# Kernel tuning notes

Hardware: AMD Instinct MI355X
Metric: run time of the kernel (lower is better)

## Reference

```python
import jax, jax.numpy as jnp
import numpy as np

PRE_NMS_TOPN = 6000   # cfg.TEST.RPN_PRE_NMS_TOP_N
POST_NMS_TOPN = 1000  # cfg.TEST.RPN_POST_NMS_TOP_N
NMS_THRESH = 0.7      # cfg.TEST.RPN_NMS_THRESH
MIN_SIZE = 0.0        # cfg.TEST.RPN_MIN_SIZE
BBOX_XFORM_CLIP = float(np.log(1000.0 / 16.0))
FEAT_STRIDE = 8.0     # 1 / spatial_scale


def _generate_anchors(base_size=16, ratios=(0.5, 1.0, 2.0), scales=(2, 4, 8, 16, 32)):
    """Standard Detectron anchor generation -> (A, 4) = (15, 4)."""
    def whctrs(a):
        w = a[2] - a[0] + 1.0
        h = a[3] - a[1] + 1.0
        return w, h, a[0] + 0.5 * (w - 1.0), a[1] + 0.5 * (h - 1.0)

    def mk(ws, hs, xc, yc):
        ws = ws[:, None]; hs = hs[:, None]
        return np.hstack([xc - 0.5 * (ws - 1.0), yc - 0.5 * (hs - 1.0),
                          xc + 0.5 * (ws - 1.0), yc + 0.5 * (hs - 1.0)])

    base = np.array([0.0, 0.0, base_size - 1.0, base_size - 1.0])
    w, h, xc, yc = whctrs(base)
    rs = np.array(ratios)
    ws = np.round(np.sqrt(w * h / rs))
    hs = np.round(ws * rs)
    ratio_anchors = mk(ws, hs, xc, yc)
    out = []
    for a in ratio_anchors:
        w, h, xc, yc = whctrs(a)
        sc = np.array(scales, dtype=np.float64)
        out.append(mk(w * sc, h * sc, xc, yc))
    return np.vstack(out).astype(np.float32)


def _proposals_one_image(all_anchors, im_info, bbox_deltas, scores):
    # bbox_deltas: (4A, H, W), scores: (A, H, W)
    deltas = bbox_deltas.transpose(1, 2, 0).reshape(-1, 4)  # (K*A, 4)
    s = scores.transpose(1, 2, 0).reshape(-1)               # (K*A,)

    # pre-NMS top-k by objectness (argpartition+argsort in original)
    top_s, order = jax.lax.top_k(s, PRE_NMS_TOPN)
    d = deltas[order]
    anc = all_anchors[order]

    # bbox_transform with weights (1,1,1,1) and dw/dh clipping
    ws = anc[:, 2] - anc[:, 0] + 1.0
    hs = anc[:, 3] - anc[:, 1] + 1.0
    cx = anc[:, 0] + 0.5 * ws
    cy = anc[:, 1] + 0.5 * hs
    dx, dy = d[:, 0], d[:, 1]
    dw = jnp.minimum(d[:, 2], BBOX_XFORM_CLIP)
    dh = jnp.minimum(d[:, 3], BBOX_XFORM_CLIP)
    pcx = dx * ws + cx
    pcy = dy * hs + cy
    pw = jnp.exp(dw) * ws
    ph = jnp.exp(dh) * hs
    x1 = pcx - 0.5 * pw
    y1 = pcy - 0.5 * ph
    x2 = pcx + 0.5 * pw - 1.0
    y2 = pcy + 0.5 * ph - 1.0

    # clip_tiled_boxes to image extent
    h_im, w_im, scale = im_info[0], im_info[1], im_info[2]
    x1 = jnp.clip(x1, 0.0, w_im - 1.0)
    y1 = jnp.clip(y1, 0.0, h_im - 1.0)
    x2 = jnp.clip(x2, 0.0, w_im - 1.0)
    y2 = jnp.clip(y2, 0.0, h_im - 1.0)
    boxes = jnp.stack([x1, y1, x2, y2], axis=1)  # (PRE, 4)

    # _filter_boxes -> validity mask (replaces gather-by-keep)
    bws = x2 - x1 + 1.0
    bhs = y2 - y1 + 1.0
    min_sz = MIN_SIZE * scale
    valid = (bws >= min_sz) & (bhs >= min_sz) & ((x1 + bws / 2.0) < w_im) & ((y1 + bhs / 2.0) < h_im)

    # greedy NMS on score-sorted boxes (boxes already sorted descending)
    areas = bws * bhs
    ix1 = jnp.maximum(x1[:, None], x1[None, :])
    iy1 = jnp.maximum(y1[:, None], y1[None, :])
    ix2 = jnp.minimum(x2[:, None], x2[None, :])
    iy2 = jnp.minimum(y2[:, None], y2[None, :])
    inter = jnp.maximum(ix2 - ix1 + 1.0, 0.0) * jnp.maximum(iy2 - iy1 + 1.0, 0.0)
    iou = inter / (areas[:, None] + areas[None, :] - inter)

    later = jnp.arange(PRE_NMS_TOPN)

    def body(i, keep):
        sup = keep[i] & (iou[i] > NMS_THRESH) & (later > i)
        return keep & ~sup

    keep = jax.lax.fori_loop(0, PRE_NMS_TOPN, body, valid)

    # fixed-size output: top POST_NMS_TOPN surviving boxes, padded (score=-1, box=0)
    masked = jnp.where(keep, top_s, -1.0)
    out_s, idx = jax.lax.top_k(masked, POST_NMS_TOPN)
    pad = (out_s > -1.0).astype(boxes.dtype)
    out_b = boxes[idx] * pad[:, None]
    return out_b, out_s


def reference(rpn_cls_prob, rpn_bbox_pred, im_info, anchors):
    N, A, H, W = rpn_cls_prob.shape
    dt = rpn_bbox_pred.dtype
    shift_x = jnp.arange(W, dtype=dt) * FEAT_STRIDE
    shift_y = jnp.arange(H, dtype=dt) * FEAT_STRIDE
    # torch.meshgrid default 'ij' ordering (faithful to original)
    sx, sy = jnp.meshgrid(shift_x, shift_y, indexing='ij')  # (W, H)
    shifts = jnp.stack([sx.ravel(), sy.ravel(), sx.ravel(), sy.ravel()], axis=1)  # (K, 4)
    all_anchors = (anchors[None, :, :] + shifts[:, None, :]).reshape(-1, 4)  # (K*A, 4)

    boxes, probs = jax.vmap(_proposals_one_image, in_axes=(None, 0, 0, 0))(
        all_anchors, im_info, rpn_bbox_pred, rpn_cls_prob)
    batch_inds = jnp.broadcast_to(jnp.arange(N, dtype=boxes.dtype)[:, None, None],
                                  (N, POST_NMS_TOPN, 1))
    rois = jnp.concatenate([batch_inds, boxes], axis=-1).reshape(-1, 5)
    return rois, probs.reshape(-1)


def setup_inputs() -> dict:
    key = jax.random.key(0)
    k1, k2 = jax.random.split(key)
    N, A, H, W = 2, 15, 128, 128
    rpn_cls_prob = jax.random.uniform(k1, (N, A, H, W), dtype=jnp.float32)
    rpn_bbox_pred = jax.random.normal(k2, (N, 4 * A, H, W), dtype=jnp.float32) * 0.2
    im_info = jnp.tile(jnp.array([[1024.0, 1024.0, 1.0]], dtype=jnp.float32), (N, 1))
    anchors = jnp.asarray(_generate_anchors())
    return {"rpn_cls_prob": rpn_cls_prob, "rpn_bbox_pred": rpn_bbox_pred,
            "im_info": im_info, "anchors": anchors}
```

## Files before the change

kernel.cpp:

```cpp
#include <hip/hip_runtime.h>
#include <hip/hip_bf16.h>

#define A_NUM 15
#define HDIM 128
#define WDIM 128
#define HW (HDIM*WDIM)
#define PER_IMG (A_NUM*HW)
#define NIMG 2
#define PRE_N 6000
#define POST_N 1000
#define NBLK 94
#define NPAD (NBLK*64)
#define SORTN 8192
#define CHUNK4 4096
#define NBIN 16384
#define HPART 16
#define PROD_T 448
#define WPT 14

typedef unsigned long long ull;

#define META_OFF   0u
#define HIST_OFF   64u
#define SEL_OFF    131136u
#define BOX_OFF    262208u
#define VALIDW_OFF 550976u
#define MASK_OFF   553024u

__device__ __forceinline__ unsigned int f2ord(float f) {
    unsigned int u = __float_as_uint(f);
    return (u & 0x80000000u) ? ~u : (u | 0x80000000u);
}
__device__ __forceinline__ float ord2f(unsigned int u) {
    unsigned int s = (u & 0x80000000u) ? (u ^ 0x80000000u) : ~u;
    return __uint_as_float(s);
}
__device__ __forceinline__ ull readlane64(ull v, int l) {
    unsigned int lo = (unsigned int)__builtin_amdgcn_readlane((int)(unsigned int)v, l);
    unsigned int hi = (unsigned int)__builtin_amdgcn_readlane((int)(unsigned int)(v >> 32), l);
    return ((ull)hi << 32) | lo;
}
__device__ __forceinline__ void barrier_lds() {
    asm volatile("s_waitcnt lgkmcnt(0)" ::: "memory");
    __builtin_amdgcn_s_barrier();
    asm volatile("" ::: "memory");
}

__global__ __launch_bounds__(1024) void k_hist16(const float* __restrict__ cls,
                                                 unsigned int* __restrict__ hist) {
    __shared__ unsigned int h[NBIN];
    int img = blockIdx.y, part = blockIdx.x;
    int t = threadIdx.x;
    for (int b = t; b < NBIN; b += 1024) h[b] = 0;
    __syncthreads();
    int base = img * PER_IMG + part * (PER_IMG / HPART);
    for (int e = t; e < PER_IMG / HPART; e += 1024) {
        unsigned int u = f2ord(cls[base + e]);
        unsigned int bin = (u >> 16) - 0x8000u;
        if (bin > (NBIN - 1)) bin = NBIN - 1;
        atomicAdd(&h[bin], 1u);
    }
    __syncthreads();
    unsigned int* hp = hist + (size_t)img * NBIN;
    for (int b = t; b < NBIN; b += 1024)
        if (h[b]) atomicAdd(&hp[b], h[b]);
}

__global__ __launch_bounds__(1024) void k_scan16(const unsigned int* __restrict__ hist,
                                                 unsigned int* __restrict__ meta) {
    __shared__ unsigned int csum[1024];
    __shared__ unsigned int aux[64];
    __shared__ unsigned int binv[16];
    int img = blockIdx.x, t = threadIdx.x;
    const unsigned int* hp = hist + (size_t)img * NBIN;
    unsigned int s = 0;
    #pragma unroll
    for (int q = 0; q < 16; ++q) s += hp[t * 16 + q];
    csum[t] = s;
    __syncthreads();
    if (t < 64) {
        unsigned int x = 0;
        #pragma unroll
        for (int q = 0; q < 16; ++q) x += csum[t * 16 + q];
        aux[t] = x;
    }
    __syncthreads();
    if (t < 64) {
        unsigned int suf = 0;
        for (int q = t; q < 64; ++q) suf += aux[q];
        ull mb1 = __ballot(suf >= PRE_N);
        int sstar = 63 - __clzll(mb1);
        unsigned int sufnext = (unsigned)__shfl((int)suf, (sstar + 1) & 63);
        unsigned int cumAbove = (sstar == 63) ? 0u : sufnext;
        unsigned int sufC = 0;
        if (t < 16) {
            for (int q = sstar * 16 + t; q < sstar * 16 + 16; ++q) sufC += csum[q];
            sufC += cumAbove;
        }
        ull mb2 = __ballot((t < 16) && (sufC >= PRE_N));
        int crel = 63 - __clzll(mb2);
        int cstar = sstar * 16 + crel;
        unsigned int cumAbove2 = (crel == 15) ? cumAbove : (unsigned)__shfl((int)sufC, crel + 1);
        if (t < 16) binv[t] = hp[cstar * 16 + t];
        unsigned int sufB = 0;
        if (t < 16) {
            for (int q = t; q < 16; ++q) sufB += binv[q];
            sufB += cumAbove2;
        }
        ull mb3 = __ballot((t < 16) && (sufB >= PRE_N));
        int brel = 63 - __clzll(mb3);
        if (t == 0) {
            meta[2 + img] = (unsigned)(cstar * 16 + brel) + 0x8000u;
            meta[img] = 0u;
        }
    }
}

__global__ __launch_bounds__(256) void k_gather(const float* __restrict__ cls,
                                                unsigned int* __restrict__ meta,
                                                ull* __restrict__ selkeys) {
    __shared__ unsigned int lcnt[NIMG], lbase[NIMG];
    int t = threadIdx.x;
    int tid = blockIdx.x * 256 + t;
    if (t < NIMG) lcnt[t] = 0;
    __syncthreads();
    unsigned int T0 = meta[2], T1 = meta[3];
    int a = tid / HW;
    int pos = tid - a * HW;
    int m = pos * A_NUM + a;
    int lane = t & 63;
    unsigned int uv[NIMG];
    bool pr[NIMG];
    unsigned int lofs[NIMG];
    #pragma unroll
    for (int img = 0; img < NIMG; ++img) {
        unsigned int T = img ? T1 : T0;
        unsigned int u = f2ord(cls[img * PER_IMG + tid]);
        uv[img] = u;
        bool pred = (u >> 16) >= T;
        pr[img] = pred;
        ull mball = __ballot((int)pred);
        unsigned int o = 0;
        if (pred) {
            int leader = __ffsll((long long)mball) - 1;
            unsigned int wbase = 0;
            if (lane == leader) wbase = atomicAdd(&lcnt[img], (unsigned)__popcll(mball));
            wbase = (unsigned)__shfl((int)wbase, leader);
            o = wbase + (unsigned)__popcll(mball & ((1ull << lane) - 1ull));
        }
        lofs[img] = o;
    }
    __syncthreads();
    if (t < NIMG) lbase[t] = atomicAdd(&meta[t], lcnt[t]);
    __syncthreads();
    #pragma unroll
    for (int img = 0; img < NIMG; ++img) {
        if (pr[img]) {
            unsigned int p = lbase[img] + lofs[img];
            if (p < SORTN)
                selkeys[(size_t)img * SORTN + p] =
                    ((ull)(~uv[img]) << 32) | (unsigned int)m;
        }
    }
}

__global__ __launch_bounds__(512) void k_sortA(ull* __restrict__ selkeys,
                                               const unsigned int* __restrict__ meta) {
    __shared__ ull key[CHUNK4];
    int img = blockIdx.x >> 1, c = blockIdx.x & 1;
    unsigned int cnt = meta[img];
    if (cnt > SORTN) cnt = SORTN;
    ull* g = selkeys + (size_t)img * SORTN;
    int base = c * CHUNK4;
    for (int i = threadIdx.x; i < CHUNK4; i += 512)
        key[i] = (base + i < (int)cnt) ? g[base + i] : ~0ull;
    __syncthreads();
    bool desc = (c & 1);
    for (int k = 2; k <= CHUNK4; k <<= 1) {
        for (int j = k >> 1; j > 0; j >>= 1) {
            for (int p = threadIdx.x; p < CHUNK4 / 2; p += 512) {
                int i = ((p & ~(j - 1)) << 1) | (p & (j - 1));
                int x = i | j;
                bool up = (((i & k) == 0) != desc);
                ull A = key[i], B = key[x];
                if ((A > B) == up) { key[i] = B; key[x] = A; }
            }
            __syncthreads();
        }
    }
    for (int i = threadIdx.x; i < CHUNK4; i += 512) g[base + i] = key[i];
}

__global__ __launch_bounds__(512) void k_sortC(ull* __restrict__ selkeys) {
    __shared__ ull key[SORTN];
    int img = blockIdx.x;
    ull* g = selkeys + (size_t)img * SORTN;
    for (int i = threadIdx.x; i < SORTN; i += 512) key[i] = g[i];
    __syncthreads();
    for (int j = SORTN / 2; j > 0; j >>= 1) {
        for (int p = threadIdx.x; p < SORTN / 2; p += 512) {
            int i = ((p & ~(j - 1)) << 1) | (p & (j - 1));
            int x = i | j;
            ull A = key[i], B = key[x];
            if (A > B) { key[i] = B; key[x] = A; }
        }
        __syncthreads();
    }
    for (int i = threadIdx.x; i < PRE_N; i += 512) g[i] = key[i];
}

__global__ void k_decode(const ull* __restrict__ selkeys,
                         const float* __restrict__ bbox, const float* __restrict__ anchors,
                         const float* __restrict__ iminfo,
                         float* __restrict__ boxsoa, ull* __restrict__ validwArr) {
    int r = blockIdx.x * blockDim.x + threadIdx.x;
    int img = blockIdx.y;
    bool in = r < PRE_N;
    int rr = in ? r : 0;
    ull keyv = selkeys[(size_t)img * SORTN + rr];
    unsigned int m = (unsigned int)(keyv & 0xFFFFFFFFu);
    unsigned int u = ~(unsigned int)(keyv >> 32);
    float score = ord2f(u);
    int q = m / A_NUM;
    int a = m - q * A_NUM;
    int w = q & (WDIM - 1);
    int h = q >> 7;
    float sx = (float)h * 8.0f;
    float sy = (float)w * 8.0f;
    float a0 = __fadd_rn(anchors[a * 4 + 0], sx);
    float a1 = __fadd_rn(anchors[a * 4 + 1], sy);
    float a2 = __fadd_rn(anchors[a * 4 + 2], sx);
    float a3 = __fadd_rn(anchors[a * 4 + 3], sy);
    float ws = __fadd_rn(__fsub_rn(a2, a0), 1.0f);
    float hs = __fadd_rn(__fsub_rn(a3, a1), 1.0f);
    float cx = __fadd_rn(a0, __fmul_rn(0.5f, ws));
    float cy = __fadd_rn(a1, __fmul_rn(0.5f, hs));
    const float* bb = bbox + (size_t)img * 4 * A_NUM * HW;
    int base = h * WDIM + w;
    float dx = bb[(a * 4 + 0) * HW + base];
    float dy = bb[(a * 4 + 1) * HW + base];
    float dwv = bb[(a * 4 + 2) * HW + base];
    float dhv = bb[(a * 4 + 3) * HW + base];
    const float CLIPV = 4.135166556742356f;
    float dw = fminf(dwv, CLIPV);
    float dh = fminf(dhv, CLIPV);
    float pcx = __fadd_rn(__fmul_rn(dx, ws), cx);
    float pcy = __fadd_rn(__fmul_rn(dy, hs), cy);
    float pw = __fmul_rn(expf(dw), ws);
    float ph = __fmul_rn(expf(dh), hs);
    float x1 = __fsub_rn(pcx, __fmul_rn(0.5f, pw));
    float y1 = __fsub_rn(pcy, __fmul_rn(0.5f, ph));
    float x2 = __fsub_rn(__fadd_rn(pcx, __fmul_rn(0.5f, pw)), 1.0f);
    float y2 = __fsub_rn(__fadd_rn(pcy, __fmul_rn(0.5f, ph)), 1.0f);
    float him = iminfo[img * 3 + 0], wim = iminfo[img * 3 + 1], scale = iminfo[img * 3 + 2];
    float wmax = __fsub_rn(wim, 1.0f), hmax = __fsub_rn(him, 1.0f);
    x1 = fminf(fmaxf(x1, 0.0f), wmax);
    y1 = fminf(fmaxf(y1, 0.0f), hmax);
    x2 = fminf(fmaxf(x2, 0.0f), wmax);
    y2 = fminf(fmaxf(y2, 0.0f), hmax);
    float bws = __fadd_rn(__fsub_rn(x2, x1), 1.0f);
    float bhs = __fadd_rn(__fsub_rn(y2, y1), 1.0f);
    float minsz = __fmul_rn(0.0f, scale);
    bool valid = (bws >= minsz) && (bhs >= minsz) &&
                 (__fadd_rn(x1, __fdiv_rn(bws, 2.0f)) < wim) &&
                 (__fadd_rn(y1, __fdiv_rn(bhs, 2.0f)) < him);
    float area = __fmul_rn(bws, bhs);
    if (in) {
        boxsoa[(0 * NIMG + img) * NPAD + r] = x1;
        boxsoa[(1 * NIMG + img) * NPAD + r] = y1;
        boxsoa[(2 * NIMG + img) * NPAD + r] = x2;
        boxsoa[(3 * NIMG + img) * NPAD + r] = y2;
        boxsoa[(4 * NIMG + img) * NPAD + r] = area;
        boxsoa[(5 * NIMG + img) * NPAD + r] = score;
    }
    ull bw = __ballot((int)(in && valid));
    if ((threadIdx.x & 63) == 0) {
        int blk = r >> 6;
        if (blk < NBLK) validwArr[img * 128 + blk] = bw;
    }
}

__global__ __launch_bounds__(256) void k_mask(const float* __restrict__ boxsoa,
                                              ull* __restrict__ Mc) {
    int cb = blockIdx.x, rbq = blockIdx.y, img = blockIdx.z;
    if ((rbq << 2) > cb) return;
    int t = threadIdx.x, wv = t >> 6, lane = t & 63;
    __shared__ float jx1[64], jy1[64], jx2[64], jy2[64], jar[64];
    const float* X1 = boxsoa + (0 * NIMG + img) * NPAD;
    const float* Y1 = boxsoa + (1 * NIMG + img) * NPAD;
    const float* X2 = boxsoa + (2 * NIMG + img) * NPAD;
    const float* Y2 = boxsoa + (3 * NIMG + img) * NPAD;
    const float* AR = boxsoa + (4 * NIMG + img) * NPAD;
    int j0 = cb * 64;
    if (t < 64) {
        int jidx = j0 + t;
        bool jin = jidx < PRE_N;
        jx1[t] = jin ? X1[jidx] : 0.0f;
        jy1[t] = jin ? Y1[jidx] : 0.0f;
        jx2[t] = jin ? X2[jidx] : 0.0f;
        jy2[t] = jin ? Y2[jidx] : 0.0f;
        jar[t] = jin ? AR[jidx] : 1.0f;
    }
    __syncthreads();
    int rb = rbq * 4 + wv;
    if (rb > cb) return;
    int r = rb * 64 + lane;
    ull bits = 0ULL;
    if (r < PRE_N) {
        float x1 = X1[r], y1 = Y1[r], x2 = X2[r], y2 = Y2[r], ai = AR[r];
        for (int jj = 0; jj < 64; ++jj) {
            int j = j0 + jj;
            if (j == r || j >= PRE_N) continue;
            float ix1 = fmaxf(x1, jx1[jj]);
            float iy1 = fmaxf(y1, jy1[jj]);
            float ix2 = fminf(x2, jx2[jj]);
            float iy2 = fminf(y2, jy2[jj]);
            float iw = fmaxf(__fadd_rn(__fsub_rn(ix2, ix1), 1.0f), 0.0f);
            float ih = fmaxf(__fadd_rn(__fsub_rn(iy2, iy1), 1.0f), 0.0f);
            float inter = __fmul_rn(iw, ih);
            float denom = __fsub_rn(__fadd_rn(ai, jar[jj]), inter);
            float iou = __fdiv_rn(inter, denom);
            if (iou > 0.7f) bits |= (1ULL << jj);
        }
    }
    Mc[((size_t)img * NBLK + cb) * NPAD + r] = bits;
}

__global__ __launch_bounds__(512, 1) void k_reduce(const ull* __restrict__ Mc,
                                                   const ull* __restrict__ validwArr,
                                                   const float* __restrict__ boxsoa,
                                                   float* __restrict__ out) {
    __shared__ ull buf[3][NPAD];
    __shared__ ull keptLDS[NBLK];
    __shared__ ull partial[8][64];
    __shared__ unsigned short s_list[POST_N];
    __shared__ int s_stop, s_cnt;
    int img = blockIdx.x;
    int tid = threadIdx.x;
    int wv = tid >> 6, lane = tid & 63;
    const ull* MCI = Mc + (size_t)img * NBLK * NPAD;
    ull vw_a = 0, vw_b = 0;
    ull rbufA[WPT], rbufB[WPT];
    #pragma unroll
    for (int q = 0; q < WPT; ++q) { rbufA[q] = 0ULL; rbufB[q] = 0ULL; }
    int pid = tid - 64;
    if (wv == 0) {
        vw_a = validwArr[img * 128 + lane];
        vw_b = (lane + 64 < NBLK) ? validwArr[img * 128 + lane + 64] : 0ULL;
        if (lane == 0) { s_stop = 0; s_cnt = 0; }
    } else {
        #pragma unroll
        for (int q = 0; q < WPT; ++q) {
            int w = pid + PROD_T * q;
            rbufA[q] = (w < 64) ? MCI[w] : 0ULL;
        }
        #pragma unroll
        for (int q = 0; q < WPT; ++q) {
            int w = pid + PROD_T * q;
            if (w < 64) buf[0][w] = rbufA[q];
        }
        #pragma unroll
        for (int q = 0; q < WPT; ++q) {
            int w = pid + PROD_T * q;
            rbufB[q] = (w < 128) ? MCI[NPAD + w] : 0ULL;
        }
        #pragma unroll
        for (int q = 0; q < WPT; ++q) {
            int w = pid + PROD_T * q;
            rbufA[q] = (w < 192) ? MCI[2 * (size_t)NPAD + w] : 0ULL;
        }
    }
    __syncthreads();
    int cnt = 0;
    for (int ib = 0; ib < NBLK; ++ib) {
        int bcur = ib % 3, bnx = (ib + 1) % 3;
        if (wv == 0) {
            ull acc = 0ULL;
            if (ib > 0) {
                #pragma unroll
                for (int q = 0; q < 8; ++q) acc |= partial[q][lane];
            }
            unsigned int lo = (unsigned)acc, hi = (unsigned)(acc >> 32);
            #pragma unroll
            for (int s2 = 1; s2 < 64; s2 <<= 1) {
                lo |= (unsigned)__shfl_xor((int)lo, s2);
                hi |= (unsigned)__shfl_xor((int)hi, s2);
            }
            ull sup = ((ull)hi << 32) | lo;
            ull validw = (ib < 64) ? readlane64(vw_a, ib) : readlane64(vw_b, ib - 64);
            ull d = buf[bcur][ib * 64 + lane];
            ull live = validw & ~sup;
            unsigned int dlo = (unsigned)d, dhi = (unsigned)(d >> 32);
            ull keptb = 0ULL;
            while (live) {
                int b = __ffsll((long long)live) - 1;
                keptb |= 1ULL << b;
                if (lane == 0) s_list[cnt] = (unsigned short)(ib * 64 + b);
                ++cnt;
                if (cnt >= POST_N) break;
                unsigned int rl = (unsigned)__builtin_amdgcn_readlane((int)dlo, b);
                unsigned int rh = (unsigned)__builtin_amdgcn_readlane((int)dhi, b);
                live &= ~(((ull)rh << 32) | rl);
                live &= ~(1ULL << b);
            }
            if (lane == 0) {
                keptLDS[ib] = keptb;
                s_cnt = cnt;
                if (cnt >= POST_N) s_stop = 1;
            }
        } else {
            int c_w = ib + 1;
            if (c_w < NBLK) {
                int Ww = (c_w + 1) * 64;
                if (Ww > NPAD) Ww = NPAD;
                if (c_w & 1) {
                    #pragma unroll
                    for (int q = 0; q < WPT; ++q) {
                        int w = pid + PROD_T * q;
                        if (w < Ww) buf[bnx][w] = rbufB[q];
                    }
                } else {
                    #pragma unroll
                    for (int q = 0; q < WPT; ++q) {
                        int w = pid + PROD_T * q;
                        if (w < Ww) buf[bnx][w] = rbufA[q];
                    }
                }
            }
            int c_l = ib + 3;
            if (c_l < NBLK) {
                int Wn = (c_l + 1) * 64;
                if (Wn > NPAD) Wn = NPAD;
                const ull* gn = MCI + (size_t)c_l * NPAD;
                if (c_l & 1) {
                    #pragma unroll
                    for (int q = 0; q < WPT; ++q) {
                        int w = pid + PROD_T * q;
                        rbufB[q] = (w < Wn) ? gn[w] : 0ULL;
                    }
                } else {
                    #pragma unroll
                    for (int q = 0; q < WPT; ++q) {
                        int w = pid + PROD_T * q;
                        rbufA[q] = (w < Wn) ? gn[w] : 0ULL;
                    }
                }
            }
        }
        barrier_lds();
        if (s_stop) break;
        if (ib + 1 < NBLK) {
            ull part = 0ULL;
            for (int u = wv; u <= ib; u += 8) {
                ull kw = keptLDS[u];
                ull v = buf[bnx][u * 64 + lane];
                part |= (0ULL - ((kw >> lane) & 1ULL)) & v;
            }
            partial[wv][lane] = part;
        }
        barrier_lds();
    }
    asm volatile("s_waitcnt vmcnt(0) lgkmcnt(0)" ::: "memory");
    __syncthreads();
    int total = s_cnt > POST_N ? POST_N : s_cnt;
    for (int k = tid; k < POST_N; k += 512) {
        float x1 = 0.0f, y1 = 0.0f, x2 = 0.0f, y2 = 0.0f, sc = -1.0f;
        if (k < total) {
            int r = (int)s_list[k];
            x1 = boxsoa[(0 * NIMG + img) * NPAD + r];
            y1 = boxsoa[(1 * NIMG + img) * NPAD + r];
            x2 = boxsoa[(2 * NIMG + img) * NPAD + r];
            y2 = boxsoa[(3 * NIMG + img) * NPAD + r];
            sc = boxsoa[(5 * NIMG + img) * NPAD + r];
        }
        float* roi = out + (size_t)(img * POST_N + k) * 5;
        roi[0] = (float)img;
        roi[1] = x1;
        roi[2] = y1;
        roi[3] = x2;
        roi[4] = y2;
        out[NIMG * POST_N * 5 + img * POST_N + k] = sc;
    }
}

extern "C" void kernel_launch(void* const* d_in, const int* in_sizes, int n_in,
                              void* d_out, int out_size, void* d_ws, size_t ws_size,
                              hipStream_t stream) {
    const float* cls = (const float*)d_in[0];
    const float* bbox = (const float*)d_in[1];
    const float* iminfo = (const float*)d_in[2];
    const float* anchors = (const float*)d_in[3];
    float* out = (float*)d_out;
    char* ws = (char*)d_ws;

    unsigned int* meta = (unsigned int*)(ws + META_OFF);
    unsigned int* hist = (unsigned int*)(ws + HIST_OFF);
    ull* selkeys = (ull*)(ws + SEL_OFF);
    float* boxsoa = (float*)(ws + BOX_OFF);
    ull* validwArr = (ull*)(ws + VALIDW_OFF);
    ull* mask = (ull*)(ws + MASK_OFF);

    hipMemsetAsync(hist, 0, (size_t)NIMG * NBIN * sizeof(unsigned int), stream);
    k_hist16<<<dim3(HPART, NIMG), 1024, 0, stream>>>(cls, hist);
    k_scan16<<<NIMG, 1024, 0, stream>>>(hist, meta);
    k_gather<<<PER_IMG / 256, 256, 0, stream>>>(cls, meta, selkeys);
    k_sortA<<<2 * NIMG, 512, 0, stream>>>(selkeys, meta);
    k_sortC<<<NIMG, 512, 0, stream>>>(selkeys);
    k_decode<<<dim3((PRE_N + 255) / 256, NIMG), 256, 0, stream>>>(selkeys, bbox, anchors, iminfo,
                                                                  boxsoa, validwArr);
    k_mask<<<dim3(NBLK, (NBLK + 3) / 4, NIMG), 256, 0, stream>>>(boxsoa, mask);
    k_reduce<<<NIMG, 512, 0, stream>>>(mask, validwArr, boxsoa, out);
}
```

Measured before the change: 264.2 us.

## Overlap suppression partial reduction with serial NMS wave, one barrier per block

Restructures the NMS reduce loop so producer waves compute the OR-reduction of kept-row masks for the next block during the current block's serial scan, instead of after a barrier. The reduction lags by one block, and wave 0 folds in the most recent kept block's contribution itself. Partial buffers are double-buffered and the prefetch distance grows by one block. This halves the barriers per iteration and takes the partial reduction off the critical path. It costs more bookkeeping and a deeper buffer rotation, with a risk of subtle ordering errors.

```diff
diff --git a/kernel.cpp b/kernel.cpp
--- a/kernel.cpp
+++ b/kernel.cpp
@@ -332,7 +332,7 @@
                                                    float* __restrict__ out) {
     __shared__ ull buf[3][NPAD];
     __shared__ ull keptLDS[NBLK];
-    __shared__ ull partial[8][64];
+    __shared__ ull partial[2][8][64];
     __shared__ unsigned short s_list[POST_N];
     __shared__ int s_stop, s_cnt;
     int img = blockIdx.x;
@@ -348,6 +348,8 @@
         vw_a = validwArr[img * 128 + lane];
         vw_b = (lane + 64 < NBLK) ? validwArr[img * 128 + lane + 64] : 0ULL;
         if (lane == 0) { s_stop = 0; s_cnt = 0; }
+        partial[0][0][lane] = 0ULL;
+        partial[1][0][lane] = 0ULL;
     } else {
         #pragma unroll
         for (int q = 0; q < WPT; ++q) {
@@ -367,18 +369,32 @@
         #pragma unroll
         for (int q = 0; q < WPT; ++q) {
             int w = pid + PROD_T * q;
+            if (w < 128) buf[1][w] = rbufB[q];
+        }
+        #pragma unroll
+        for (int q = 0; q < WPT; ++q) {
+            int w = pid + PROD_T * q;
             rbufA[q] = (w < 192) ? MCI[2 * (size_t)NPAD + w] : 0ULL;
         }
+        #pragma unroll
+        for (int q = 0; q < WPT; ++q) {
+            int w = pid + PROD_T * q;
+            rbufB[q] = (w < 256) ? MCI[3 * (size_t)NPAD + w] : 0ULL;
+        }
+        partial[0][wv][lane] = 0ULL;
+        partial[1][wv][lane] = 0ULL;
     }
     __syncthreads();
     int cnt = 0;
     for (int ib = 0; ib < NBLK; ++ib) {
-        int bcur = ib % 3, bnx = (ib + 1) % 3;
+        int bcur = ib % 3, bn1 = (ib + 1) % 3, bn2 = (ib + 2) % 3;
         if (wv == 0) {
             ull acc = 0ULL;
             if (ib > 0) {
                 #pragma unroll
-                for (int q = 0; q < 8; ++q) acc |= partial[q][lane];
+                for (int q = 1; q < 8; ++q) acc |= partial[ib & 1][q][lane];
+                ull kwp = keptLDS[ib - 1];
+                acc |= (0ULL - ((kwp >> lane) & 1ULL)) & buf[bcur][(ib - 1) * 64 + lane];
             }
             unsigned int lo = (unsigned)acc, hi = (unsigned)(acc >> 32);
             #pragma unroll
@@ -409,30 +425,30 @@
                 if (cnt >= POST_N) s_stop = 1;
             }
         } else {
-            int c_w = ib + 1;
+            int c_w = ib + 2;
             if (c_w < NBLK) {
                 int Ww = (c_w + 1) * 64;
                 if (Ww > NPAD) Ww = NPAD;
-                if (c_w & 1) {
+                if (ib & 1) {
                     #pragma unroll
                     for (int q = 0; q < WPT; ++q) {
                         int w = pid + PROD_T * q;
-                        if (w < Ww) buf[bnx][w] = rbufB[q];
+                        if (w < Ww) buf[bn2][w] = rbufB[q];
                     }
                 } else {
                     #pragma unroll
                     for (int q = 0; q < WPT; ++q) {
                         int w = pid + PROD_T * q;
-                        if (w < Ww) buf[bnx][w] = rbufA[q];
+                        if (w < Ww) buf[bn2][w] = rbufA[q];
                     }
                 }
             }
-            int c_l = ib + 3;
+            int c_l = ib + 4;
             if (c_l < NBLK) {
                 int Wn = (c_l + 1) * 64;
                 if (Wn > NPAD) Wn = NPAD;
                 const ull* gn = MCI + (size_t)c_l * NPAD;
-                if (c_l & 1) {
+                if (ib & 1) {
                     #pragma unroll
                     for (int q = 0; q < WPT; ++q) {
                         int w = pid + PROD_T * q;
@@ -446,19 +462,18 @@
                     }
                 }
             }
+            if (ib + 1 < NBLK) {
+                ull part = 0ULL;
+                for (int u = wv - 1; u <= ib - 1; u += 7) {
+                    ull kw = keptLDS[u];
+                    ull v = buf[bn1][u * 64 + lane];
+                    part |= (0ULL - ((kw >> lane) & 1ULL)) & v;
+                }
+                partial[(ib + 1) & 1][wv][lane] = part;
+            }
         }
         barrier_lds();
         if (s_stop) break;
-        if (ib + 1 < NBLK) {
-            ull part = 0ULL;
-            for (int u = wv; u <= ib; u += 8) {
-                ull kw = keptLDS[u];
-                ull v = buf[bnx][u * 64 + lane];
-                part |= (0ULL - ((kw >> lane) & 1ULL)) & v;
-            }
-            partial[wv][lane] = part;
-        }
-        barrier_lds();
     }
     asm volatile("s_waitcnt vmcnt(0) lgkmcnt(0)" ::: "memory");
     __syncthreads();
```

Result: faster. 258.6 us (-2.1%).
